# Optimization experiments

Hardware: AMD Instinct MI355X
Metric: run time of the kernel (lower is better)

The kernel has to match this reference:

```python
import jax, jax.numpy as jnp
import numpy as np

B, T, S, E, H, V = 64, 32, 64, 128, 256, 32000


def setup_inputs() -> dict:
    key = jax.random.key(0)
    ks = jax.random.split(key, 13)
    n = lambda k, sh, s=1.0: jax.random.normal(k, sh, dtype=jnp.float32) * s
    return {
        "target": n(ks[0], (B, T, E)),
        "inp": n(ks[1], (B, T, E)),
        "pos_feature": n(ks[2], (B, E)),
        "encoder_state": n(ks[3], (B, H)),
        "encoder_output": n(ks[4], (B, S, 2 * H)),
        "W_ih": n(ks[5], (3 * H, 3 * E + H), 0.05),
        "W_hh": n(ks[6], (3 * H, H), 0.05),
        "b_ih": n(ks[7], (3 * H,), 0.05),
        "b_hh": n(ks[8], (3 * H,), 0.05),
        "Win_w": n(ks[9], (2 * H, H), 0.05),
        "Win_b": n(ks[10], (2 * H,), 0.05),
        "Wout_w": n(ks[11], (V, 3 * H), 0.05),
        "Wout_b": n(ks[12], (V,), 0.05),
    }


def reference(target, inp, pos_feature, encoder_state, encoder_output,
              W_ih, W_hh, b_ih, b_hh, Win_w, Win_b, Wout_w, Wout_b):
    bsz = target.shape[0]
    hdim = W_hh.shape[1]

    def gru_cell(x, h):
        gi = x @ W_ih.T + b_ih          # [B, 3H]
        gh = h @ W_hh.T + b_hh          # [B, 3H]
        i_r, i_z, i_n = jnp.split(gi, 3, axis=1)
        h_r, h_z, h_n = jnp.split(gh, 3, axis=1)
        r = jax.nn.sigmoid(i_r + h_r)
        z = jax.nn.sigmoid(i_z + h_z)
        n = jnp.tanh(i_n + r * h_n)
        return (1.0 - z) * n + z * h

    def step(hs, xs):
        dec_in, in_t = xs                                   # [B,E], [B,E]
        x = jnp.concatenate([dec_in, pos_feature, encoder_state, in_t], axis=1)
        hs = gru_cell(x, hs)
        q = hs @ Win_w.T + Win_b                            # [B, 2H]
        attn = jnp.einsum('bsd,bd->bs', encoder_output, q)  # [B, S]
        score = jax.nn.softmax(attn, axis=1)
        h_star = jnp.einsum('bs,bsd->bd', score, encoder_output)  # [B, 2H]
        feat = jnp.concatenate([h_star, hs], axis=1)        # [B, 3H]
        out = jax.nn.log_softmax(jax.nn.relu(feat @ Wout_w.T + Wout_b), axis=1)
        return hs, out

    hs0 = jnp.zeros((bsz, hdim), dtype=target.dtype)
    xs = (jnp.swapaxes(target, 0, 1), jnp.swapaxes(inp, 0, 1))  # time-major
    hs, outputs = jax.lax.scan(step, hs0, xs)
    return hs, outputs  # hs: [B,H], outputs: [T,B,V]
```

## Files before the change

### kernel.cpp

```cpp
#include <hip/hip_runtime.h>
#include <hip/hip_bf16.h>


typedef __attribute__((ext_vector_type(8))) short  s8v;
typedef __attribute__((ext_vector_type(8))) __bf16 bf8v;
typedef __attribute__((ext_vector_type(4))) float  f4v;
typedef __attribute__((ext_vector_type(2))) float  f2v;

#define DEV static __device__ __forceinline__

DEV ushort f2b(float f) {
  unsigned u = __float_as_uint(f);
  u += 0x7fffu + ((u >> 16) & 1u);
  return (ushort)(u >> 16);
}
DEV float b2fs(short s) { return __uint_as_float(((unsigned)(ushort)s) << 16); }

__global__ __launch_bounds__(256) void k_gather(
    const float* __restrict__ target, const float* __restrict__ inp,
    const float* __restrict__ posf,   const float* __restrict__ encs,
    ushort* __restrict__ X) {
  int tb = blockIdx.x; int t = tb >> 6, b = tb & 63;
  size_t xrow = (size_t)tb * 640;
  for (int c = threadIdx.x; c < 640; c += 256) {
    float v;
    if (c < 128)      v = target[((size_t)b * 32 + t) * 128 + c];
    else if (c < 256) v = posf[(size_t)b * 128 + (c - 128)];
    else if (c < 512) v = encs[(size_t)b * 256 + (c - 256)];
    else              v = inp[((size_t)b * 32 + t) * 128 + (c - 512)];
    X[xrow + c] = f2b(v);
  }
}

template <bool RELU>
__global__ __launch_bounds__(256) void k_gemm_bt(
    const ushort* __restrict__ A, const float* __restrict__ B,
    const float* __restrict__ bias, float* __restrict__ Out,
    int N, int K) {
  __shared__ __align__(16) ushort As[128 * 40];
  __shared__ __align__(16) ushort Bs[128 * 40];
  const int m0 = blockIdx.x * 128, n0 = blockIdx.y * 128;
  const int tid = threadIdx.x;
  const int lane = tid & 63, wv = tid >> 6;
  const int wm = (wv >> 1) * 64, wn = (wv & 1) * 64;
  const int fr = lane & 15, fq = lane >> 4;
  const int srow = tid >> 2, scol = (tid & 3) * 8;
  f4v acc[4][4];
#pragma unroll
  for (int i = 0; i < 4; ++i)
#pragma unroll
    for (int j = 0; j < 4; ++j) acc[i][j] = {0.f, 0.f, 0.f, 0.f};
  const ushort* ag = A + (size_t)(m0 + srow) * K + scol;
  const float*  bg = B + (size_t)(n0 + srow) * K + scol;
  for (int k0 = 0; k0 < K; k0 += 32) {
    s8v a0 = *(const s8v*)(ag + k0);
    s8v a1 = *(const s8v*)(ag + k0 + (size_t)64 * K);
    f4v b00 = *(const f4v*)(bg + k0);
    f4v b01 = *(const f4v*)(bg + k0 + 4);
    f4v b10 = *(const f4v*)(bg + k0 + (size_t)64 * K);
    f4v b11 = *(const f4v*)(bg + k0 + (size_t)64 * K + 4);
    s8v b0, b1;
#pragma unroll
    for (int u = 0; u < 4; ++u) {
      b0[u]     = (short)f2b(b00[u]);
      b0[u + 4] = (short)f2b(b01[u]);
      b1[u]     = (short)f2b(b10[u]);
      b1[u + 4] = (short)f2b(b11[u]);
    }
    __syncthreads();
    *(s8v*)&As[srow * 40 + scol] = a0;
    *(s8v*)&As[(srow + 64) * 40 + scol] = a1;
    *(s8v*)&Bs[srow * 40 + scol] = b0;
    *(s8v*)&Bs[(srow + 64) * 40 + scol] = b1;
    __syncthreads();
    bf8v af[4], bfr[4];
#pragma unroll
    for (int i = 0; i < 4; ++i)
      af[i] = *(const bf8v*)&As[(wm + i * 16 + fr) * 40 + fq * 8];
#pragma unroll
    for (int j = 0; j < 4; ++j)
      bfr[j] = *(const bf8v*)&Bs[(wn + j * 16 + fr) * 40 + fq * 8];
#pragma unroll
    for (int i = 0; i < 4; ++i)
#pragma unroll
      for (int j = 0; j < 4; ++j)
        acc[i][j] = __builtin_amdgcn_mfma_f32_16x16x32_bf16(af[i], bfr[j],
                                                            acc[i][j], 0, 0, 0);
  }
  float bj[4];
#pragma unroll
  for (int j = 0; j < 4; ++j) bj[j] = bias[n0 + wn + j * 16 + fr];
#pragma unroll
  for (int i = 0; i < 4; ++i) {
#pragma unroll
    for (int j = 0; j < 4; ++j) {
#pragma unroll
      for (int r = 0; r < 4; ++r) {
        int gm = m0 + wm + i * 16 + fq * 4 + r;
        int gn = n0 + wn + j * 16 + fr;
        float v = acc[i][j][r] + bj[j];
        if (RELU) v = fmaxf(v, 0.f);
        Out[(size_t)gm * N + gn] = v;
      }
    }
  }
}

__global__ __launch_bounds__(256) void k_recur(
    const float* __restrict__ gi_all,
    const float* __restrict__ eo,
    const float* __restrict__ Whh,
    const float* __restrict__ bhh,
    const float* __restrict__ Winw,
    const float* __restrict__ Winb,
    ushort* __restrict__ feat,
    float* __restrict__ hs_out) {
  const int b = blockIdx.x, t = threadIdx.x;
  __shared__ __align__(16) float h[256];
  __shared__ __align__(16) float q[512];
  __shared__ float attnp[64][4];
  __shared__ float score[64];
  const float* eoB = eo + (size_t)b * 32768;
  const float bhr = bhh[t], bhz = bhh[t + 256], bhn = bhh[t + 512];
  const float qb0 = Winb[t], qb1 = Winb[t + 256];
  const float* wr = Whh + t * 256;
  const float* wz = Whh + (t + 256) * 256;
  const float* wn = Whh + (t + 512) * 256;
  const float* w0 = Winw + t * 256;
  const float* w1 = Winw + (t + 256) * 256;
  h[t] = 0.f;
  __syncthreads();
  for (int st = 0; st < 32; ++st) {
    const float* gi = gi_all + ((size_t)st * 64 + b) * 768;
    float ar = bhr, az = bhz, an = bhn;
#pragma unroll 4
    for (int k = 0; k < 256; k += 8) {
      f4v ha = *(const f4v*)&h[k];
      f4v hb = *(const f4v*)&h[k + 4];
      f4v r0 = *(const f4v*)(wr + k), r1 = *(const f4v*)(wr + k + 4);
      f4v z0 = *(const f4v*)(wz + k), z1 = *(const f4v*)(wz + k + 4);
      f4v n0 = *(const f4v*)(wn + k), n1 = *(const f4v*)(wn + k + 4);
      float hv[8] = {ha.x, ha.y, ha.z, ha.w, hb.x, hb.y, hb.z, hb.w};
      float rv[8] = {r0.x, r0.y, r0.z, r0.w, r1.x, r1.y, r1.z, r1.w};
      float zv[8] = {z0.x, z0.y, z0.z, z0.w, z1.x, z1.y, z1.z, z1.w};
      float nv[8] = {n0.x, n0.y, n0.z, n0.w, n1.x, n1.y, n1.z, n1.w};
#pragma unroll
      for (int u = 0; u < 8; ++u) {
        ar = fmaf(hv[u], rv[u], ar);
        az = fmaf(hv[u], zv[u], az);
        an = fmaf(hv[u], nv[u], an);
      }
    }
    float r = 1.f / (1.f + __expf(-(gi[t] + ar)));
    float z = 1.f / (1.f + __expf(-(gi[t + 256] + az)));
    float e2 = __expf(2.f * (gi[t + 512] + r * an));
    float n = 1.f - 2.f / (e2 + 1.f);
    float hnew = (1.f - z) * n + z * h[t];
    __syncthreads();
    h[t] = hnew;
    __syncthreads();
    float a0 = qb0, a1 = qb1;
#pragma unroll 4
    for (int k = 0; k < 256; k += 8) {
      f4v ha = *(const f4v*)&h[k];
      f4v hb = *(const f4v*)&h[k + 4];
      f4v u00 = *(const f4v*)(w0 + k), u01 = *(const f4v*)(w0 + k + 4);
      f4v u10 = *(const f4v*)(w1 + k), u11 = *(const f4v*)(w1 + k + 4);
      float hv[8] = {ha.x, ha.y, ha.z, ha.w, hb.x, hb.y, hb.z, hb.w};
      float v0[8] = {u00.x, u00.y, u00.z, u00.w, u01.x, u01.y, u01.z, u01.w};
      float v1[8] = {u10.x, u10.y, u10.z, u10.w, u11.x, u11.y, u11.z, u11.w};
#pragma unroll
      for (int u = 0; u < 8; ++u) {
        a0 = fmaf(hv[u], v0[u], a0);
        a1 = fmaf(hv[u], v1[u], a1);
      }
    }
    q[t] = a0;
    q[t + 256] = a1;
    __syncthreads();
    {
      int s = t >> 2, p = t & 3;
      const float* ep = eoB + s * 512 + p * 128;
      const float* qp = &q[p * 128];
      float aa = 0.f;
#pragma unroll 4
      for (int dc = 0; dc < 128; dc += 8) {
        f4v e0 = *(const f4v*)(ep + dc), e1 = *(const f4v*)(ep + dc + 4);
        f4v q0 = *(const f4v*)(qp + dc), q1 = *(const f4v*)(qp + dc + 4);
        aa = fmaf(q0.x, e0.x, aa); aa = fmaf(q0.y, e0.y, aa);
        aa = fmaf(q0.z, e0.z, aa); aa = fmaf(q0.w, e0.w, aa);
        aa = fmaf(q1.x, e1.x, aa); aa = fmaf(q1.y, e1.y, aa);
        aa = fmaf(q1.z, e1.z, aa); aa = fmaf(q1.w, e1.w, aa);
      }
      attnp[s][p] = aa;
    }
    __syncthreads();
    if (t < 64) {
      float a = attnp[t][0] + attnp[t][1] + attnp[t][2] + attnp[t][3];
      float m = a;
#pragma unroll
      for (int off = 32; off > 0; off >>= 1) m = fmaxf(m, __shfl_xor(m, off));
      float e = __expf(a - m);
      float ss = e;
#pragma unroll
      for (int off = 32; off > 0; off >>= 1) ss += __shfl_xor(ss, off);
      score[t] = e / ss;
    }
    __syncthreads();
    {
      int d0 = 2 * t;
      float s0 = 0.f, s1 = 0.f;
#pragma unroll 8
      for (int s2 = 0; s2 < 64; ++s2) {
        float sc = score[s2];
        f2v ev = *(const f2v*)(eoB + s2 * 512 + d0);
        s0 = fmaf(sc, ev.x, s0);
        s1 = fmaf(sc, ev.y, s1);
      }
      size_t row = ((size_t)st * 64 + b) * 768;
      feat[row + d0] = f2b(s0);
      feat[row + d0 + 1] = f2b(s1);
      feat[row + 512 + t] = f2b(h[t]);
    }
    __syncthreads();
  }
  hs_out[(size_t)b * 256 + t] = h[t];
}

__global__ __launch_bounds__(256) void k_logsm(float* __restrict__ out) {
  float* p = out + (size_t)blockIdx.x * 32000;
  const int t = threadIdx.x;
  __shared__ float red[4];
  float m = 0.f;
  for (int c = t; c < 4000; c += 256) {
    f4v a = *(const f4v*)(p + (size_t)c * 8);
    f4v b = *(const f4v*)(p + (size_t)c * 8 + 4);
    m = fmaxf(m, fmaxf(fmaxf(a.x, a.y), fmaxf(a.z, a.w)));
    m = fmaxf(m, fmaxf(fmaxf(b.x, b.y), fmaxf(b.z, b.w)));
  }
#pragma unroll
  for (int off = 32; off > 0; off >>= 1) m = fmaxf(m, __shfl_xor(m, off));
  if ((t & 63) == 0) red[t >> 6] = m;
  __syncthreads();
  m = fmaxf(fmaxf(red[0], red[1]), fmaxf(red[2], red[3]));
  float s = 0.f;
  for (int c = t; c < 4000; c += 256) {
    f4v a = *(const f4v*)(p + (size_t)c * 8);
    f4v b = *(const f4v*)(p + (size_t)c * 8 + 4);
    s += __expf(a.x - m) + __expf(a.y - m) + __expf(a.z - m) + __expf(a.w - m);
    s += __expf(b.x - m) + __expf(b.y - m) + __expf(b.z - m) + __expf(b.w - m);
  }
#pragma unroll
  for (int off = 32; off > 0; off >>= 1) s += __shfl_xor(s, off);
  __syncthreads();
  if ((t & 63) == 0) red[t >> 6] = s;
  __syncthreads();
  s = red[0] + red[1] + red[2] + red[3];
  const float L = m + logf(s);
  for (int c = t; c < 4000; c += 256) {
    f4v a = *(const f4v*)(p + (size_t)c * 8);
    f4v b = *(const f4v*)(p + (size_t)c * 8 + 4);
    a.x -= L; a.y -= L; a.z -= L; a.w -= L;
    b.x -= L; b.y -= L; b.z -= L; b.w -= L;
    *(f4v*)(p + (size_t)c * 8) = a;
    *(f4v*)(p + (size_t)c * 8 + 4) = b;
  }
}

extern "C" void kernel_launch(void* const* d_in, const int* in_sizes, int n_in,
                              void* d_out, int out_size, void* d_ws, size_t ws_size,
                              hipStream_t stream) {
  (void)in_sizes; (void)n_in; (void)out_size; (void)ws_size;
  const float* target = (const float*)d_in[0];
  const float* inp    = (const float*)d_in[1];
  const float* posf   = (const float*)d_in[2];
  const float* encs   = (const float*)d_in[3];
  const float* enco   = (const float*)d_in[4];
  const float* Wih    = (const float*)d_in[5];
  const float* Whh    = (const float*)d_in[6];
  const float* bih    = (const float*)d_in[7];
  const float* bhh    = (const float*)d_in[8];
  const float* Winw   = (const float*)d_in[9];
  const float* Winb   = (const float*)d_in[10];
  const float* Woutw  = (const float*)d_in[11];
  const float* Woutb  = (const float*)d_in[12];

  char* ws = (char*)d_ws;
  ushort* X    = (ushort*)(ws);
  float*  gi   = (float*)(ws + 0x300000);
  ushort* feat = (ushort*)(ws + 0x900000);
  float* hs    = (float*)d_out;
  float* logits = hs + 16384;

  k_gather<<<2048, 256, 0, stream>>>(target, inp, posf, encs, X);
  k_gemm_bt<false><<<dim3(16, 6), 256, 0, stream>>>(X, Wih, bih, gi, 768, 640);
  k_recur<<<64, 256, 0, stream>>>(gi, enco, Whh, bhh, Winw, Winb, feat, hs);
  k_gemm_bt<true><<<dim3(16, 250), 256, 0, stream>>>(feat, Woutw, Woutb, logits,
                                                     32000, 768);
  k_logsm<<<2048, 256, 0, stream>>>(logits);
}
```

Baseline: 2.050 ms.

## Widen recurrent kernel to 1024 threads with split-K and bf16 recurrent weights

Converts W_hh and Win_w to bf16 in a new pre-pass kernel so the recurrent kernel streams half the weight bytes on every step. The recurrence block grows from 256 to 1024 threads: the gate and query matvecs are split across K with partial sums reduced in shared memory, and the attention dot and context sum are spread across more threads using shuffles and a two-way split. The hidden state is double-buffered. This targets the latency-bound serial loop that uses only 64 blocks, at the cost of more shared memory, more barriers and bf16 rounding in the recurrent weights.

```diff
diff --git a/kernel.cpp b/kernel.cpp
--- a/kernel.cpp
+++ b/kernel.cpp
@@ -5,7 +5,6 @@
 typedef __attribute__((ext_vector_type(8))) short  s8v;
 typedef __attribute__((ext_vector_type(8))) __bf16 bf8v;
 typedef __attribute__((ext_vector_type(4))) float  f4v;
-typedef __attribute__((ext_vector_type(2))) float  f2v;
 
 #define DEV static __device__ __forceinline__
 
@@ -30,6 +29,17 @@
     else              v = inp[((size_t)b * 32 + t) * 128 + (c - 512)];
     X[xrow + c] = f2b(v);
   }
+}
+
+__global__ __launch_bounds__(256) void k_cvt(
+    const float* __restrict__ Whh, const float* __restrict__ Winw,
+    ushort* __restrict__ Whh_b, ushort* __restrict__ Winw_b) {
+  size_t j = ((size_t)blockIdx.x * 256 + threadIdx.x) * 4;
+  const float* src; ushort* dst;
+  if (j < 196608) { src = Whh + j; dst = Whh_b + j; }
+  else            { src = Winw + (j - 196608); dst = Winw_b + (j - 196608); }
+  f4v v = *(const f4v*)src;
+  dst[0] = f2b(v.x); dst[1] = f2b(v.y); dst[2] = f2b(v.z); dst[3] = f2b(v.w);
 }
 
 template <bool RELU>
@@ -106,125 +116,139 @@
   }
 }
 
-__global__ __launch_bounds__(256) void k_recur(
+__global__ __launch_bounds__(1024) void k_recur(
     const float* __restrict__ gi_all,
     const float* __restrict__ eo,
-    const float* __restrict__ Whh,
+    const ushort* __restrict__ Whh_b,
     const float* __restrict__ bhh,
-    const float* __restrict__ Winw,
+    const ushort* __restrict__ Winw_b,
     const float* __restrict__ Winb,
     ushort* __restrict__ feat,
     float* __restrict__ hs_out) {
-  const int b = blockIdx.x, t = threadIdx.x;
-  __shared__ __align__(16) float h[256];
-  __shared__ __align__(16) float q[512];
-  __shared__ float attnp[64][4];
+  const int b = blockIdx.x, tid = threadIdx.x;
+  __shared__ __align__(16) float h[2][256];
+  __shared__ __align__(16) float qv[512];
+  __shared__ __align__(16) float gis[768];
+  __shared__ __align__(16) float part[4][3][256];
+  __shared__ __align__(16) float qpart[2][512];
+  __shared__ __align__(16) float hpart[2][512];
+  __shared__ float attns[64];
   __shared__ float score[64];
   const float* eoB = eo + (size_t)b * 32768;
-  const float bhr = bhh[t], bhz = bhh[t + 256], bhn = bhh[t + 512];
-  const float qb0 = Winb[t], qb1 = Winb[t + 256];
-  const float* wr = Whh + t * 256;
-  const float* wz = Whh + (t + 256) * 256;
-  const float* wn = Whh + (t + 512) * 256;
-  const float* w0 = Winw + t * 256;
-  const float* w1 = Winw + (t + 256) * 256;
-  h[t] = 0.f;
+
+  float bhr = 0.f, bhz = 0.f, bhn = 0.f, qb = 0.f;
+  if (tid < 256) { bhr = bhh[tid]; bhz = bhh[tid + 256]; bhn = bhh[tid + 512]; }
+  if (tid < 512) qb = Winb[tid];
+  if (tid < 256) h[0][tid] = 0.f;
   __syncthreads();
+
+  const int o = tid & 255, p = tid >> 8;
+  const int o2 = tid & 511, p2 = tid >> 9;
+  const int s16 = tid >> 4, g16 = tid & 15;
+  const ushort* wr = Whh_b + (size_t)o * 256 + p * 64;
+  const ushort* wz = wr + 256 * 256;
+  const ushort* wn = wr + 512 * 256;
+  const ushort* w0 = Winw_b + (size_t)o2 * 256 + p2 * 128;
+
   for (int st = 0; st < 32; ++st) {
-    const float* gi = gi_all + ((size_t)st * 64 + b) * 768;
-    float ar = bhr, az = bhz, an = bhn;
-#pragma unroll 4
-    for (int k = 0; k < 256; k += 8) {
-      f4v ha = *(const f4v*)&h[k];
-      f4v hb = *(const f4v*)&h[k + 4];
-      f4v r0 = *(const f4v*)(wr + k), r1 = *(const f4v*)(wr + k + 4);
-      f4v z0 = *(const f4v*)(wz + k), z1 = *(const f4v*)(wz + k + 4);
-      f4v n0 = *(const f4v*)(wn + k), n1 = *(const f4v*)(wn + k + 4);
-      float hv[8] = {ha.x, ha.y, ha.z, ha.w, hb.x, hb.y, hb.z, hb.w};
-      float rv[8] = {r0.x, r0.y, r0.z, r0.w, r1.x, r1.y, r1.z, r1.w};
-      float zv[8] = {z0.x, z0.y, z0.z, z0.w, z1.x, z1.y, z1.z, z1.w};
-      float nv[8] = {n0.x, n0.y, n0.z, n0.w, n1.x, n1.y, n1.z, n1.w};
-#pragma unroll
-      for (int u = 0; u < 8; ++u) {
-        ar = fmaf(hv[u], rv[u], ar);
-        az = fmaf(hv[u], zv[u], az);
-        an = fmaf(hv[u], nv[u], an);
+    const float* hc = h[st & 1];
+    float* hn = h[(st & 1) ^ 1];
+    const float* gi_row = gi_all + ((size_t)st * 64 + b) * 768;
+    float gpre = (tid < 768) ? gi_row[tid] : 0.f;
+
+    {
+      float ar = 0.f, az = 0.f, an = 0.f;
+      const float* hcb = &hc[p * 64];
+#pragma unroll
+      for (int k = 0; k < 64; k += 8) {
+        s8v r8 = *(const s8v*)(wr + k);
+        s8v z8 = *(const s8v*)(wz + k);
+        s8v n8 = *(const s8v*)(wn + k);
+        f4v h0 = *(const f4v*)(hcb + k);
+        f4v h1 = *(const f4v*)(hcb + k + 4);
+        float hv[8] = {h0.x, h0.y, h0.z, h0.w, h1.x, h1.y, h1.z, h1.w};
+#pragma unroll
+        for (int u = 0; u < 8; ++u) {
+          ar = fmaf(hv[u], b2fs(r8[u]), ar);
+          az = fmaf(hv[u], b2fs(z8[u]), az);
+          an = fmaf(hv[u], b2fs(n8[u]), an);
+        }
       }
-    }
-    float r = 1.f / (1.f + __expf(-(gi[t] + ar)));
-    float z = 1.f / (1.f + __expf(-(gi[t + 256] + az)));
-    float e2 = __expf(2.f * (gi[t + 512] + r * an));
-    float n = 1.f - 2.f / (e2 + 1.f);
-    float hnew = (1.f - z) * n + z * h[t];
-    __syncthreads();
-    h[t] = hnew;
-    __syncthreads();
-    float a0 = qb0, a1 = qb1;
-#pragma unroll 4
-    for (int k = 0; k < 256; k += 8) {
-      f4v ha = *(const f4v*)&h[k];
-      f4v hb = *(const f4v*)&h[k + 4];
-      f4v u00 = *(const f4v*)(w0 + k), u01 = *(const f4v*)(w0 + k + 4);
-      f4v u10 = *(const f4v*)(w1 + k), u11 = *(const f4v*)(w1 + k + 4);
-      float hv[8] = {ha.x, ha.y, ha.z, ha.w, hb.x, hb.y, hb.z, hb.w};
-      float v0[8] = {u00.x, u00.y, u00.z, u00.w, u01.x, u01.y, u01.z, u01.w};
-      float v1[8] = {u10.x, u10.y, u10.z, u10.w, u11.x, u11.y, u11.z, u11.w};
-#pragma unroll
-      for (int u = 0; u < 8; ++u) {
-        a0 = fmaf(hv[u], v0[u], a0);
-        a1 = fmaf(hv[u], v1[u], a1);
+      part[p][0][o] = ar; part[p][1][o] = az; part[p][2][o] = an;
+    }
+    if (tid < 768) gis[tid] = gpre;
+    __syncthreads();
+    if (tid < 256) {
+      float ar = part[0][0][tid] + part[1][0][tid] + part[2][0][tid] + part[3][0][tid] + bhr;
+      float az = part[0][1][tid] + part[1][1][tid] + part[2][1][tid] + part[3][1][tid] + bhz;
+      float an = part[0][2][tid] + part[1][2][tid] + part[2][2][tid] + part[3][2][tid] + bhn;
+      float r = 1.f / (1.f + __expf(-(gis[tid] + ar)));
+      float z = 1.f / (1.f + __expf(-(gis[tid + 256] + az)));
+      float e2 = __expf(2.f * (gis[tid + 512] + r * an));
+      float n = 1.f - 2.f / (e2 + 1.f);
+      float hnew = (1.f - z) * n + z * hc[tid];
+      hn[tid] = hnew;
+      if (st == 31) hs_out[(size_t)b * 256 + tid] = hnew;
+    }
+    __syncthreads();
+    {
+      float a0 = 0.f;
+      const float* hb = &hn[p2 * 128];
+#pragma unroll
+      for (int k = 0; k < 128; k += 8) {
+        s8v u8 = *(const s8v*)(w0 + k);
+        f4v h0 = *(const f4v*)(hb + k);
+        f4v h1 = *(const f4v*)(hb + k + 4);
+        float hv[8] = {h0.x, h0.y, h0.z, h0.w, h1.x, h1.y, h1.z, h1.w};
+#pragma unroll
+        for (int u = 0; u < 8; ++u) a0 = fmaf(hv[u], b2fs(u8[u]), a0);
       }
-    }
-    q[t] = a0;
-    q[t + 256] = a1;
-    __syncthreads();
-    {
-      int s = t >> 2, p = t & 3;
-      const float* ep = eoB + s * 512 + p * 128;
-      const float* qp = &q[p * 128];
+      qpart[p2][o2] = a0;
+    }
+    __syncthreads();
+    if (tid < 512) qv[tid] = qpart[0][tid] + qpart[1][tid] + qb;
+    __syncthreads();
+    {
+      const float* ep = eoB + s16 * 512 + g16 * 4;
       float aa = 0.f;
-#pragma unroll 4
-      for (int dc = 0; dc < 128; dc += 8) {
-        f4v e0 = *(const f4v*)(ep + dc), e1 = *(const f4v*)(ep + dc + 4);
-        f4v q0 = *(const f4v*)(qp + dc), q1 = *(const f4v*)(qp + dc + 4);
-        aa = fmaf(q0.x, e0.x, aa); aa = fmaf(q0.y, e0.y, aa);
-        aa = fmaf(q0.z, e0.z, aa); aa = fmaf(q0.w, e0.w, aa);
-        aa = fmaf(q1.x, e1.x, aa); aa = fmaf(q1.y, e1.y, aa);
-        aa = fmaf(q1.z, e1.z, aa); aa = fmaf(q1.w, e1.w, aa);
+#pragma unroll
+      for (int j = 0; j < 8; ++j) {
+        f4v e4 = *(const f4v*)(ep + j * 64);
+        f4v q4 = *(const f4v*)(&qv[g16 * 4 + j * 64]);
+        aa = fmaf(e4.x, q4.x, aa); aa = fmaf(e4.y, q4.y, aa);
+        aa = fmaf(e4.z, q4.z, aa); aa = fmaf(e4.w, q4.w, aa);
       }
-      attnp[s][p] = aa;
-    }
-    __syncthreads();
-    if (t < 64) {
-      float a = attnp[t][0] + attnp[t][1] + attnp[t][2] + attnp[t][3];
-      float m = a;
+      aa += __shfl_xor(aa, 8); aa += __shfl_xor(aa, 4);
+      aa += __shfl_xor(aa, 2); aa += __shfl_xor(aa, 1);
+      if (g16 == 0) attns[s16] = aa;
+    }
+    __syncthreads();
+    if (tid < 64) {
+      float a = attns[tid], m = a;
 #pragma unroll
       for (int off = 32; off > 0; off >>= 1) m = fmaxf(m, __shfl_xor(m, off));
-      float e = __expf(a - m);
-      float ss = e;
+      float e = __expf(a - m), ss = e;
 #pragma unroll
       for (int off = 32; off > 0; off >>= 1) ss += __shfl_xor(ss, off);
-      score[t] = e / ss;
-    }
-    __syncthreads();
-    {
-      int d0 = 2 * t;
-      float s0 = 0.f, s1 = 0.f;
+      score[tid] = e / ss;
+    }
+    __syncthreads();
+    {
+      const float* ep = eoB + (size_t)p2 * 32 * 512 + o2;
+      const float* sc = &score[p2 * 32];
+      float a = 0.f;
 #pragma unroll 8
-      for (int s2 = 0; s2 < 64; ++s2) {
-        float sc = score[s2];
-        f2v ev = *(const f2v*)(eoB + s2 * 512 + d0);
-        s0 = fmaf(sc, ev.x, s0);
-        s1 = fmaf(sc, ev.y, s1);
-      }
+      for (int s2 = 0; s2 < 32; ++s2) a = fmaf(sc[s2], ep[(size_t)s2 * 512], a);
+      hpart[p2][o2] = a;
+    }
+    __syncthreads();
+    {
       size_t row = ((size_t)st * 64 + b) * 768;
-      feat[row + d0] = f2b(s0);
-      feat[row + d0 + 1] = f2b(s1);
-      feat[row + 512 + t] = f2b(h[t]);
-    }
-    __syncthreads();
-  }
-  hs_out[(size_t)b * 256 + t] = h[t];
+      if (tid < 512)      feat[row + tid] = f2b(hpart[0][tid] + hpart[1][tid]);
+      else if (tid < 768) feat[row + tid] = f2b(hn[tid - 512]);
+    }
+    __syncthreads();
+  }
 }
 
 __global__ __launch_bounds__(256) void k_logsm(float* __restrict__ out) {
@@ -286,15 +310,18 @@
   const float* Woutb  = (const float*)d_in[12];
 
   char* ws = (char*)d_ws;
-  ushort* X    = (ushort*)(ws);
-  float*  gi   = (float*)(ws + 0x300000);
-  ushort* feat = (ushort*)(ws + 0x900000);
+  ushort* X      = (ushort*)(ws);
+  float*  gi     = (float*)(ws + 0x280000);
+  ushort* feat   = (ushort*)(ws + 0x880000);
+  ushort* Whh_b  = (ushort*)(ws + 0xB80000);
+  ushort* Winw_b = (ushort*)(ws + 0xBE0000);
   float* hs    = (float*)d_out;
   float* logits = hs + 16384;
 
+  k_cvt<<<320, 256, 0, stream>>>(Whh, Winw, Whh_b, Winw_b);
   k_gather<<<2048, 256, 0, stream>>>(target, inp, posf, encs, X);
   k_gemm_bt<false><<<dim3(16, 6), 256, 0, stream>>>(X, Wih, bih, gi, 768, 640);
-  k_recur<<<64, 256, 0, stream>>>(gi, enco, Whh, bhh, Winw, Winb, feat, hs);
+  k_recur<<<64, 1024, 0, stream>>>(gi, enco, Whh_b, bhh, Winw_b, Winb, feat, hs);
   k_gemm_bt<true><<<dim3(16, 250), 256, 0, stream>>>(feat, Woutw, Woutb, logits,
                                                      32000, 768);
   k_logsm<<<2048, 256, 0, stream>>>(logits);
```

Result: slower. 3.373 ms (+64.5%).
